# Kernel tuning notes

Measured on AMD Instinct MI355X. Metric: run time of the kernel, lower is better.

Reference implementation:

```python
import jax, jax.numpy as jnp
import numpy as np

EMBED_DIM = 2048
NUM_HEADS = 16
B, L = 1, 4096


def setup_inputs() -> dict:
    key = jax.random.key(0)
    ks = jax.random.split(key, 6)
    s = 1.0 / np.sqrt(EMBED_DIM)
    return {
        "hidden_states": jax.random.normal(ks[0], (B, L, EMBED_DIM), jnp.float32),
        "Wq": jax.random.normal(ks[1], (EMBED_DIM, EMBED_DIM), jnp.float32) * s,
        "bq": jnp.zeros((EMBED_DIM,), jnp.float32),
        "Wk": jax.random.normal(ks[2], (EMBED_DIM, EMBED_DIM), jnp.float32) * s,
        "bk": jnp.zeros((EMBED_DIM,), jnp.float32),
        "Wv": jax.random.normal(ks[3], (EMBED_DIM, EMBED_DIM), jnp.float32) * s,
        "bv": jnp.zeros((EMBED_DIM,), jnp.float32),
        "Wo": jax.random.normal(ks[4], (EMBED_DIM, EMBED_DIM), jnp.float32) * s,
        "bo": jnp.zeros((EMBED_DIM,), jnp.float32),
        "is_causal": 1,
    }


def reference(hidden_states, Wq, bq, Wk, bk, Wv, bv, Wo, bo, is_causal):
    Bc, Lc, D = hidden_states.shape
    H = NUM_HEADS
    Dh = D // H
    scale = Dh ** (-0.5)

    def proj(W, b):
        # torch Linear: x @ W.T + b; reshape to [B, H, L, Dh]
        y = jnp.einsum('bld,ed->ble', hidden_states, W) + b
        return y.reshape(Bc, Lc, H, Dh).transpose(0, 2, 1, 3)

    q = proj(Wq, bq)
    k = proj(Wk, bk)
    v = proj(Wv, bv)

    scores = jnp.einsum('bhqd,bhkd->bhqk', q, k) * scale  # [B,H,L,L]
    if is_causal:
        causal = jnp.triu(jnp.ones((Lc, Lc), dtype=bool), k=1)
        scores = jnp.where(causal, -jnp.inf, scores)
    w = jax.nn.softmax(scores, axis=-1)
    attn = jnp.einsum('bhqk,bhkd->bhqd', w, v)
    attn = attn.transpose(0, 2, 1, 3).reshape(Bc, Lc, D)
    return jnp.einsum('bld,ed->ble', attn, Wo) + bo
```

## Files before the change

### kernel.cpp

```cpp
#include <hip/hip_runtime.h>
#include <hip/hip_bf16.h>

typedef unsigned short u16;
typedef unsigned int u32;
typedef __attribute__((ext_vector_type(8))) short short8;
typedef __attribute__((ext_vector_type(4))) float f32x4;

#define L 4096
#define DMODEL 2048
#define NHEADS 16
#define DHEAD 128
#define QSCALE (0.08838834764831845f * 1.44269504088896340f)

__device__ __forceinline__ u16 f2bf(float f){
  union { float f; unsigned int i; } v; v.f = f;
  unsigned int u = v.i;
  u += 0x7fffu + ((u >> 16) & 1u);
  return (u16)(u >> 16);
}

__device__ __forceinline__ u32 cvtpk(float lo, float hi){
  u32 d;
  asm("v_cvt_pk_bf16_f32 %0, %1, %2" : "=v"(d) : "v"(lo), "v"(hi));
  return d;
}

__global__ void cast_all_kernel(const float* __restrict__ X, u16* __restrict__ Xo,
                                const float* __restrict__ w0, const float* __restrict__ w1,
                                const float* __restrict__ w2, const float* __restrict__ w3,
                                u16* __restrict__ o0, u16* __restrict__ o1,
                                u16* __restrict__ o2, u16* __restrict__ o3){
  const int y = blockIdx.y;
  const float* in = (y == 0) ? X : (y == 1) ? w0 : (y == 2) ? w1 : (y == 3) ? w2 : w3;
  u16* out = (y == 0) ? Xo : (y == 1) ? o0 : (y == 2) ? o1 : (y == 3) ? o2 : o3;
  const int n = (y == 0) ? (L * DMODEL) : (DMODEL * DMODEL);
  int stride = gridDim.x * blockDim.x * 4;
  for (int j = (blockIdx.x * blockDim.x + threadIdx.x) * 4; j < n; j += stride){
    float4 f = *reinterpret_cast<const float4*>(in + j);
    ushort4 o;
    o.x = f2bf(f.x); o.y = f2bf(f.y); o.z = f2bf(f.z); o.w = f2bf(f.w);
    *reinterpret_cast<ushort4*>(out + j) = o;
  }
}

__device__ __forceinline__ void gl_lds16(void* lds, const void* g){
  __builtin_amdgcn_global_load_lds(
      (const __attribute__((address_space(1))) unsigned int*)g,
      (__attribute__((address_space(3))) unsigned int*)lds, 16, 0, 0);
}

#define GBUF (24576)

__global__ __launch_bounds__(512, 2) void gemm_qkv(const u16* __restrict__ A,
    const u16* __restrict__ Wq, const u16* __restrict__ Wk, const u16* __restrict__ Wv,
    const float* __restrict__ bq, const float* __restrict__ bk, const float* __restrict__ bv,
    u16* __restrict__ Qb, u16* __restrict__ Kb, u16* __restrict__ Vtb){
  extern __shared__ u16 gsm[];
  const int tid = threadIdx.x;
  const int wid = tid >> 6, lane = tid & 63;
  const int wm = wid >> 2, wn = wid & 3;
  const int g = lane >> 4, r = lane & 15;
  const int bx = blockIdx.x;
  const int sel = blockIdx.y >> 4;
  const int byl = blockIdx.y & 15;

  const u16* W      = (sel == 0) ? Wq : (sel == 1) ? Wk : Wv;
  const float* bias = (sel == 0) ? bq : (sel == 1) ? bk : bv;
  const float cscale = (sel == 0) ? QSCALE : 1.0f;

  const int srow = tid >> 3;
  const int sc = ((tid & 7) * 16) ^ ((srow & 7) << 4);
  const u16* Ag = A + ((size_t)(bx * 256) + srow) * DMODEL + (sc >> 1);
  const u16* Bg = W + ((size_t)(byl * 128) + srow) * DMODEL + (sc >> 1);
  const int ldsw = wid * 1024;

  f32x4 acc[8][2];
  #pragma unroll
  for (int m = 0; m < 8; ++m){ acc[m][0] = (f32x4){0,0,0,0}; acc[m][1] = (f32x4){0,0,0,0}; }

  const int NK = DMODEL / 64;

  auto STAGE = [&](int b, int tk){
    char* ab = (char*)(gsm + b * GBUF);
    char* bb = (char*)(gsm + b * GBUF + 16384);
    const int ke = tk * 64;
    #pragma unroll
    for (int i = 0; i < 4; ++i)
      gl_lds16(ab + i * 8192 + ldsw, (const char*)(Ag + (size_t)i * 64 * DMODEL + ke));
    #pragma unroll
    for (int i = 0; i < 2; ++i)
      gl_lds16(bb + i * 8192 + ldsw, (const char*)(Bg + (size_t)i * 64 * DMODEL + ke));
  };

  STAGE(0, 0); STAGE(1, 1);

  for (int t = 0; t < NK; ++t){
    if (t < NK - 1) asm volatile("s_waitcnt vmcnt(6)" ::: "memory");
    else            asm volatile("s_waitcnt vmcnt(0)" ::: "memory");
    __builtin_amdgcn_sched_barrier(0);
    __builtin_amdgcn_s_barrier();
    __builtin_amdgcn_sched_barrier(0);

    if (t + 2 < NK) STAGE((t + 2) % 3, t + 2);

    const char* ab = (const char*)(gsm + (t % 3) * GBUF);
    const char* bb = (const char*)(gsm + (t % 3) * GBUF + 16384);

    short8 af[8][2], bf[2][2];
    #pragma unroll
    for (int mt = 0; mt < 8; ++mt){
      const int ar = wm * 128 + mt * 16 + r;
      #pragma unroll
      for (int ks = 0; ks < 2; ++ks)
        af[mt][ks] = *reinterpret_cast<const short8*>(
            ab + ar * 128 + ((ks * 64 + g * 16) ^ ((ar & 7) << 4)));
    }
    #pragma unroll
    for (int nt = 0; nt < 2; ++nt){
      const int br = wn * 32 + nt * 16 + r;
      #pragma unroll
      for (int ks = 0; ks < 2; ++ks)
        bf[nt][ks] = *reinterpret_cast<const short8*>(
            bb + br * 128 + ((ks * 64 + g * 16) ^ ((br & 7) << 4)));
    }

    __builtin_amdgcn_s_setprio(1);
    #pragma unroll
    for (int mt = 0; mt < 8; ++mt)
      #pragma unroll
      for (int nt = 0; nt < 2; ++nt)
        #pragma unroll
        for (int ks = 0; ks < 2; ++ks)
          acc[mt][nt] = __builtin_amdgcn_mfma_f32_16x16x32_bf16(af[mt][ks], bf[nt][ks], acc[mt][nt], 0, 0, 0);
    __builtin_amdgcn_s_setprio(0);
  }

  #pragma unroll
  for (int nt = 0; nt < 2; ++nt){
    const int col = byl * 128 + wn * 32 + nt * 16 + r;
    const float bv = bias[col];
    #pragma unroll
    for (int mt = 0; mt < 8; ++mt){
      #pragma unroll
      for (int qi = 0; qi < 4; ++qi){
        const int row = bx * 256 + wm * 128 + mt * 16 + g * 4 + qi;
        const u16 hb = f2bf((acc[mt][nt][qi] + bv) * cscale);
        if (sel < 2){
          u16* outp = (sel == 0) ? Qb : Kb;
          outp[(size_t)(col >> 7) * (L * DHEAD) + (size_t)row * DHEAD + (col & 127)] = hb;
        } else {
          Vtb[(size_t)(col >> 7) * (DHEAD * L) + (size_t)(col & 127) * L + row] = hb;
        }
      }
    }
  }
}

__global__ __launch_bounds__(512, 2) void gemm_o(const u16* __restrict__ A, const u16* __restrict__ W,
                                                 const float* __restrict__ bias, float* __restrict__ outp){
  extern __shared__ u16 gsm[];
  const int tid = threadIdx.x;
  const int wid = tid >> 6, lane = tid & 63;
  const int wm = wid >> 2, wn = wid & 3;
  const int g = lane >> 4, r = lane & 15;
  const int bx = blockIdx.x, by = blockIdx.y;

  const int srow = tid >> 3;
  const int sc = ((tid & 7) * 16) ^ ((srow & 7) << 4);
  const u16* Ag = A + ((size_t)(bx * 256) + srow) * DMODEL + (sc >> 1);
  const u16* Bg = W + ((size_t)(by * 128) + srow) * DMODEL + (sc >> 1);
  const int ldsw = wid * 1024;

  f32x4 acc[8][2];
  #pragma unroll
  for (int m = 0; m < 8; ++m){ acc[m][0] = (f32x4){0,0,0,0}; acc[m][1] = (f32x4){0,0,0,0}; }

  const int NK = DMODEL / 64;

  auto STAGE = [&](int b, int tk){
    char* ab = (char*)(gsm + b * GBUF);
    char* bb = (char*)(gsm + b * GBUF + 16384);
    const int ke = tk * 64;
    #pragma unroll
    for (int i = 0; i < 4; ++i)
      gl_lds16(ab + i * 8192 + ldsw, (const char*)(Ag + (size_t)i * 64 * DMODEL + ke));
    #pragma unroll
    for (int i = 0; i < 2; ++i)
      gl_lds16(bb + i * 8192 + ldsw, (const char*)(Bg + (size_t)i * 64 * DMODEL + ke));
  };

  STAGE(0, 0); STAGE(1, 1);

  for (int t = 0; t < NK; ++t){
    if (t < NK - 1) asm volatile("s_waitcnt vmcnt(6)" ::: "memory");
    else            asm volatile("s_waitcnt vmcnt(0)" ::: "memory");
    __builtin_amdgcn_sched_barrier(0);
    __builtin_amdgcn_s_barrier();
    __builtin_amdgcn_sched_barrier(0);

    if (t + 2 < NK) STAGE((t + 2) % 3, t + 2);

    const char* ab = (const char*)(gsm + (t % 3) * GBUF);
    const char* bb = (const char*)(gsm + (t % 3) * GBUF + 16384);

    short8 af[8][2], bf[2][2];
    #pragma unroll
    for (int mt = 0; mt < 8; ++mt){
      const int ar = wm * 128 + mt * 16 + r;
      #pragma unroll
      for (int ks = 0; ks < 2; ++ks)
        af[mt][ks] = *reinterpret_cast<const short8*>(
            ab + ar * 128 + ((ks * 64 + g * 16) ^ ((ar & 7) << 4)));
    }
    #pragma unroll
    for (int nt = 0; nt < 2; ++nt){
      const int br = wn * 32 + nt * 16 + r;
      #pragma unroll
      for (int ks = 0; ks < 2; ++ks)
        bf[nt][ks] = *reinterpret_cast<const short8*>(
            bb + br * 128 + ((ks * 64 + g * 16) ^ ((br & 7) << 4)));
    }

    __builtin_amdgcn_s_setprio(1);
    #pragma unroll
    for (int mt = 0; mt < 8; ++mt)
      #pragma unroll
      for (int nt = 0; nt < 2; ++nt)
        #pragma unroll
        for (int ks = 0; ks < 2; ++ks)
          acc[mt][nt] = __builtin_amdgcn_mfma_f32_16x16x32_bf16(af[mt][ks], bf[nt][ks], acc[mt][nt], 0, 0, 0);
    __builtin_amdgcn_s_setprio(0);
  }

  #pragma unroll
  for (int nt = 0; nt < 2; ++nt){
    const int col = by * 128 + wn * 32 + nt * 16 + r;
    const float bv = bias[col];
    #pragma unroll
    for (int mt = 0; mt < 8; ++mt){
      #pragma unroll
      for (int qi = 0; qi < 4; ++qi){
        const int row = bx * 256 + wm * 128 + mt * 16 + g * 4 + qi;
        outp[(size_t)row * DMODEL + col] = acc[mt][nt][qi] + bv;
      }
    }
  }
}


__device__ __forceinline__ void stage_K64(u16* buf, const u16* Kh, int kv0, int wid, int lane){
  #pragma unroll
  for (int i = 0; i < 4; ++i){
    int ib = (wid * 4 + i) * 1024;
    int off = ib + lane * 16;
    int row = off >> 8;
    int c = off & 255;
    int sc = c ^ ((row & 7) << 4);
    gl_lds16((char*)buf + ib, (const char*)(Kh + (size_t)(kv0 + row) * DHEAD) + sc);
  }
}

__device__ __forceinline__ void stage_V64(u16* buf, const u16* Vh, int kv0, int wid, int lane){
  #pragma unroll
  for (int i = 0; i < 4; ++i){
    int ib = (wid * 4 + i) * 1024;
    int off = ib + lane * 16;
    int row = off >> 7;
    int c = off & 127;
    int sc = c ^ ((row & 7) << 4);
    gl_lds16((char*)buf + ib, (const char*)(Vh + (size_t)row * L + kv0) + sc);
  }
}

__device__ __forceinline__ void sm_R(f32x4 (&s)[4], float &l, bool dg, int qrow,
                                     int kv0, int g, u32 (&paw)[2][4]){
  if (dg){
    #pragma unroll
    for (int cb = 0; cb < 4; ++cb){
      int kvb = kv0 + cb * 16 + g * 4;
      #pragma unroll
      for (int e = 0; e < 4; ++e)
        if (kvb + e > qrow) s[cb][e] = -1e30f;
    }
  }
  float rs = 0.f;
  u32 pk[4][2];
  #pragma unroll
  for (int cb = 0; cb < 4; ++cb){
    float p0 = __builtin_amdgcn_exp2f(s[cb][0]);
    float p1 = __builtin_amdgcn_exp2f(s[cb][1]);
    float p2 = __builtin_amdgcn_exp2f(s[cb][2]);
    float p3 = __builtin_amdgcn_exp2f(s[cb][3]);
    rs += (p0 + p1) + (p2 + p3);
    pk[cb][0] = cvtpk(p0, p1);
    pk[cb][1] = cvtpk(p2, p3);
  }
  rs += __shfl_xor(rs, 16);
  rs += __shfl_xor(rs, 32);
  l += rs;
  #pragma unroll
  for (int ks = 0; ks < 2; ++ks){
    #pragma unroll
    for (int h = 0; h < 2; ++h){
      u32 a = pk[ks * 2][h], b = pk[ks * 2 + 1][h];
      asm volatile("v_permlane32_swap_b32 %0, %1" : "+v"(a), "+v"(b));
      asm volatile("v_permlane16_swap_b32 %0, %1" : "+v"(a), "+v"(b));
      paw[ks][h] = a;
      paw[ks][2 + h] = b;
    }
  }
}

__global__ __launch_bounds__(256, 2) void attn_kernel(const u16* __restrict__ Q, const u16* __restrict__ Km,
                                                      const u16* __restrict__ Vt, u16* __restrict__ Ob,
                                                      const int* __restrict__ is_causal_p){
  extern __shared__ u16 smem[];
  u16* Ks  = smem;
  u16* Vsm = smem + 16384;

  const int lane = threadIdx.x & 63, wid = threadIdx.x >> 6;
  const int g = lane >> 4, r = lane & 15;

  int lg = (blockIdx.x & 7) * 64 + (blockIdx.x >> 3);
  int head = lg >> 5;
  int raw = lg & 31;
  int j = (head & 1) ? (31 - raw) : raw;
  const int jA = j, jB = 63 - j;
  const int causal = *is_causal_p;
  const int nt = causal ? (jB + 1) : 64;

  const u16* Qh = Q  + (size_t)head * L * DHEAD;
  const u16* Kh = Km + (size_t)head * L * DHEAD;
  const u16* Vh = Vt + (size_t)head * DHEAD * L;

  const int rowA = 64 * jA + wid * 16;
  const int rowB = 64 * jB + wid * 16;

  short8 qf[2][4];
  #pragma unroll
  for (int kb = 0; kb < 4; ++kb){
    qf[0][kb] = *reinterpret_cast<const short8*>(&Qh[(size_t)(rowA + r) * DHEAD + kb * 32 + g * 8]);
    qf[1][kb] = *reinterpret_cast<const short8*>(&Qh[(size_t)(rowB + r) * DHEAD + kb * 32 + g * 8]);
  }

  f32x4 o[2][8];
  #pragma unroll
  for (int m = 0; m < 2; ++m)
    #pragma unroll
    for (int db = 0; db < 8; ++db) o[m][db] = (f32x4){0.f, 0.f, 0.f, 0.f};
  float lA = 0.f, lB = 0.f;

  stage_K64(Ks,  Kh, 0, wid, lane);
  stage_V64(Vsm, Vh, 0, wid, lane);

  for (int t = 0; t < nt; ++t){
    const int kv0 = t * 64;
    const bool actA = (!causal) || (t <= jA);
    const bool dgA = causal && (t == jA);
    const bool dgB = causal && (t == jB);

    asm volatile("s_waitcnt vmcnt(0)" ::: "memory");
    __builtin_amdgcn_sched_barrier(0);
    __builtin_amdgcn_s_barrier();
    __builtin_amdgcn_sched_barrier(0);

    if (t + 1 < nt){
      stage_K64(Ks  + ((t + 1) & 1) * 8192, Kh, kv0 + 64, wid, lane);
      stage_V64(Vsm + ((t + 1) & 1) * 8192, Vh, kv0 + 64, wid, lane);
    }

    const char* Kb = (const char*)(Ks  + (t & 1) * 8192);
    const char* Vb = (const char*)(Vsm + (t & 1) * 8192);

    f32x4 s[2][4];
    #pragma unroll
    for (int m = 0; m < 2; ++m)
      #pragma unroll
      for (int cb = 0; cb < 4; ++cb) s[m][cb] = (f32x4){-16.f, -16.f, -16.f, -16.f};
    __builtin_amdgcn_s_setprio(1);
    #pragma unroll
    for (int cb = 0; cb < 4; ++cb){
      const int rr = cb * 16 + r;
      short8 kf[4];
      #pragma unroll
      for (int kb = 0; kb < 4; ++kb)
        kf[kb] = *reinterpret_cast<const short8*>(
            Kb + rr * 256 + ((kb * 64 + g * 16) ^ ((rr & 7) << 4)));
      if (actA){
        #pragma unroll
        for (int kb = 0; kb < 4; ++kb)
          s[0][cb] = __builtin_amdgcn_mfma_f32_16x16x32_bf16(kf[kb], qf[0][kb], s[0][cb], 0, 0, 0);
      }
      #pragma unroll
      for (int kb = 0; kb < 4; ++kb)
        s[1][cb] = __builtin_amdgcn_mfma_f32_16x16x32_bf16(kf[kb], qf[1][kb], s[1][cb], 0, 0, 0);
    }
    __builtin_amdgcn_s_setprio(0);

    u32 pawA[2][4], pawB[2][4];
    if (actA) sm_R(s[0], lA, dgA, rowA + r, kv0, g, pawA);
    sm_R(s[1], lB, dgB, rowB + r, kv0, g, pawB);

    __builtin_amdgcn_s_setprio(1);
    #pragma unroll
    for (int st = 0; st < 2; ++st){
      union { u32 u[4]; short8 v; } pa0, pa1;
      #pragma unroll
      for (int w = 0; w < 4; ++w){ pa0.u[w] = pawA[st][w]; pa1.u[w] = pawB[st][w]; }
      #pragma unroll
      for (int db = 0; db < 8; ++db){
        const int rv = db * 16 + r;
        short8 vf = *reinterpret_cast<const short8*>(
            Vb + rv * 128 + (((st * 32 + g * 8) * 2) ^ ((rv & 7) << 4)));
        if (actA)
          o[0][db] = __builtin_amdgcn_mfma_f32_16x16x32_bf16(pa0.v, vf, o[0][db], 0, 0, 0);
        o[1][db] = __builtin_amdgcn_mfma_f32_16x16x32_bf16(pa1.v, vf, o[1][db], 0, 0, 0);
      }
    }
    __builtin_amdgcn_s_setprio(0);
  }

  #pragma unroll
  for (int m = 0; m < 2; ++m){
    const int rbase = m ? rowB : rowA;
    const float lv = m ? lB : lA;
    float lb[4];
    #pragma unroll
    for (int qi = 0; qi < 4; ++qi) lb[qi] = __shfl(lv, g * 4 + qi);
    #pragma unroll
    for (int db = 0; db < 8; ++db)
      #pragma unroll
      for (int qi = 0; qi < 4; ++qi){
        float val = o[m][db][qi] / lb[qi];
        int qrow = rbase + g * 4 + qi;
        Ob[(size_t)qrow * DMODEL + head * DHEAD + db * 16 + r] = f2bf(val);
      }
  }
}

extern "C" void kernel_launch(void* const* d_in, const int* in_sizes, int n_in,
                              void* d_out, int out_size, void* d_ws, size_t ws_size,
                              hipStream_t stream){
  const float* X  = (const float*)d_in[0];
  const float* Wq = (const float*)d_in[1];
  const float* bq = (const float*)d_in[2];
  const float* Wk = (const float*)d_in[3];
  const float* bk = (const float*)d_in[4];
  const float* Wv = (const float*)d_in[5];
  const float* bv = (const float*)d_in[6];
  const float* Wo = (const float*)d_in[7];
  const float* bo = (const float*)d_in[8];
  const int*   isc = (const int*)d_in[9];

  char* ws = (char*)d_ws;
  u16* Xb  = (u16*)(ws);
  u16* Qb  = (u16*)(ws + 16777216);
  u16* Kb  = (u16*)(ws + 33554432);
  u16* Vtb = (u16*)(ws + 50331648);
  u16* Wqb = (u16*)(ws + 67108864);
  u16* Wkb = (u16*)(ws + 75497472);
  u16* Wvb = (u16*)(ws + 83886080);
  u16* Wob = (u16*)(ws + 92274688);
  u16* Ob  = Xb;

  (void)hipFuncSetAttribute(reinterpret_cast<const void*>(attn_kernel),
                            hipFuncAttributeMaxDynamicSharedMemorySize, 65536);
  (void)hipFuncSetAttribute(reinterpret_cast<const void*>(gemm_qkv),
                            hipFuncAttributeMaxDynamicSharedMemorySize, 147456);
  (void)hipFuncSetAttribute(reinterpret_cast<const void*>(gemm_o),
                            hipFuncAttributeMaxDynamicSharedMemorySize, 147456);

  cast_all_kernel<<<dim3(1024, 5), 256, 0, stream>>>(X, Xb, Wq, Wk, Wv, Wo,
                                                     Wqb, Wkb, Wvb, Wob);

  gemm_qkv<<<dim3(16, 48), 512, 147456, stream>>>(Xb, Wqb, Wkb, Wvb, bq, bk, bv, Qb, Kb, Vtb);

  attn_kernel<<<512, 256, 65536, stream>>>(Qb, Kb, Vtb, Ob, isc);

  gemm_o<<<dim3(16, 16), 512, 147456, stream>>>(Ob, Wob, bo, (float*)d_out);
}
```

Measured before the change: 293.1 us.

## Retile projection GEMMs to 128x128 tiles with K=32 and block swizzle

Replaces the 256x128 tile, 512-thread, K=64 GEMMs for the QKV and output projections with a shared templated 128x128 tile, 256-thread, K=32 kernel. It uses a three-stage pipeline in about 48KB of LDS and remaps block IDs so that each group of 8 consecutive blocks is spread across the grid, aiming for better L2 locality across XCDs. The goal is more blocks and higher occupancy (launch bounds 256,3) for a better wave count on the GPU. The cost is lower per-block data reuse, more loop iterations with barriers, and a narrower LDS swizzle that may cause bank conflicts.

```diff
diff --git a/kernel.cpp b/kernel.cpp
--- a/kernel.cpp
+++ b/kernel.cpp
@@ -49,202 +49,135 @@
       (__attribute__((address_space(3))) unsigned int*)lds, 16, 0, 0);
 }
 
-#define GBUF (24576)
-
-__global__ __launch_bounds__(512, 2) void gemm_qkv(const u16* __restrict__ A,
+#define GBUF 8192
+
+template<int MODE>
+__device__ __forceinline__ void gemm128(const u16* __restrict__ A, const u16* __restrict__ W,
+                                        const float* __restrict__ bias, void* __restrict__ outp,
+                                        float cscale, int bx, int by, u16* gsm){
+  const int tid = threadIdx.x;
+  const int wid = tid >> 6, lane = tid & 63;
+  const int wm = wid >> 1, wn = wid & 1;
+  const int g = lane >> 4, r = lane & 15;
+
+  const int srow = tid >> 2;
+  const int sc = ((tid & 3) * 16) ^ (((srow >> 1) & 3) << 4);
+  const u16* Ag = A + ((size_t)(bx * 128) + srow) * DMODEL + (sc >> 1);
+  const u16* Bg = W + ((size_t)(by * 128) + srow) * DMODEL + (sc >> 1);
+
+  f32x4 acc[4][4];
+  #pragma unroll
+  for (int m = 0; m < 4; ++m)
+    #pragma unroll
+    for (int n = 0; n < 4; ++n) acc[m][n] = (f32x4){0,0,0,0};
+
+  const int NK = DMODEL / 32;
+
+  auto STAGE = [&](int b, int tk){
+    char* ab = (char*)(gsm + b * GBUF);
+    char* bb = (char*)(gsm + b * GBUF + 4096);
+    const int ke = tk * 32;
+    #pragma unroll
+    for (int i = 0; i < 2; ++i)
+      gl_lds16(ab + i * 4096 + tid * 16 - lane * 16 + lane * 16 - tid * 16 + tid * 16,
+               (const char*)(Ag + (size_t)(i * 64) * DMODEL + ke));
+    #pragma unroll
+    for (int i = 0; i < 2; ++i)
+      gl_lds16(bb + i * 4096 + tid * 16,
+               (const char*)(Bg + (size_t)(i * 64) * DMODEL + ke));
+  };
+
+  STAGE(0, 0); STAGE(1, 1);
+
+  int cur = 0;
+  for (int t = 0; t < NK; ++t){
+    if (t < NK - 1) asm volatile("s_waitcnt vmcnt(4)" ::: "memory");
+    else            asm volatile("s_waitcnt vmcnt(0)" ::: "memory");
+    __builtin_amdgcn_sched_barrier(0);
+    __builtin_amdgcn_s_barrier();
+    __builtin_amdgcn_sched_barrier(0);
+
+    if (t + 2 < NK){
+      int nb = cur + 2; if (nb >= 3) nb -= 3;
+      STAGE(nb, t + 2);
+    }
+
+    const char* ab = (const char*)(gsm + cur * GBUF);
+    const char* bb = (const char*)(gsm + cur * GBUF + 4096);
+
+    short8 af[4], bf[4];
+    #pragma unroll
+    for (int mt = 0; mt < 4; ++mt){
+      const int ar = wm * 64 + mt * 16 + r;
+      af[mt] = *reinterpret_cast<const short8*>(
+          ab + ar * 64 + ((g * 16) ^ (((ar >> 1) & 3) << 4)));
+    }
+    #pragma unroll
+    for (int nt = 0; nt < 4; ++nt){
+      const int br = wn * 64 + nt * 16 + r;
+      bf[nt] = *reinterpret_cast<const short8*>(
+          bb + br * 64 + ((g * 16) ^ (((br >> 1) & 3) << 4)));
+    }
+
+    __builtin_amdgcn_s_setprio(1);
+    #pragma unroll
+    for (int mt = 0; mt < 4; ++mt)
+      #pragma unroll
+      for (int nt = 0; nt < 4; ++nt)
+        acc[mt][nt] = __builtin_amdgcn_mfma_f32_16x16x32_bf16(af[mt], bf[nt], acc[mt][nt], 0, 0, 0);
+    __builtin_amdgcn_s_setprio(0);
+
+    ++cur; if (cur == 3) cur = 0;
+  }
+
+  #pragma unroll
+  for (int nt = 0; nt < 4; ++nt){
+    const int col = by * 128 + wn * 64 + nt * 16 + r;
+    const float bv = bias[col & (DMODEL - 1)];
+    #pragma unroll
+    for (int mt = 0; mt < 4; ++mt){
+      #pragma unroll
+      for (int qi = 0; qi < 4; ++qi){
+        const int row = bx * 128 + wm * 64 + mt * 16 + g * 4 + qi;
+        if (MODE == 0){
+          ((u16*)outp)[(size_t)((col & (DMODEL-1)) >> 7) * (L * DHEAD) + (size_t)row * DHEAD + (col & 127)]
+              = f2bf((acc[mt][nt][qi] + bv) * cscale);
+        } else if (MODE == 1){
+          ((u16*)outp)[(size_t)((col & (DMODEL-1)) >> 7) * (DHEAD * L) + (size_t)(col & 127) * L + row]
+              = f2bf(acc[mt][nt][qi] + bv);
+        } else {
+          ((float*)outp)[(size_t)row * DMODEL + col] = acc[mt][nt][qi] + bv;
+        }
+      }
+    }
+  }
+}
+
+__global__ __launch_bounds__(256, 3) void gemm_qkv(const u16* __restrict__ A,
     const u16* __restrict__ Wq, const u16* __restrict__ Wk, const u16* __restrict__ Wv,
     const float* __restrict__ bq, const float* __restrict__ bk, const float* __restrict__ bv,
     u16* __restrict__ Qb, u16* __restrict__ Kb, u16* __restrict__ Vtb){
   extern __shared__ u16 gsm[];
-  const int tid = threadIdx.x;
-  const int wid = tid >> 6, lane = tid & 63;
-  const int wm = wid >> 2, wn = wid & 3;
-  const int g = lane >> 4, r = lane & 15;
-  const int bx = blockIdx.x;
-  const int sel = blockIdx.y >> 4;
-  const int byl = blockIdx.y & 15;
-
+  int id = blockIdx.x;
+  int nid = (id & 7) * 192 + (id >> 3);
+  int by = nid >> 5, bx = nid & 31;
+  int sel = by >> 4, byl = by & 15;
   const u16* W      = (sel == 0) ? Wq : (sel == 1) ? Wk : Wv;
   const float* bias = (sel == 0) ? bq : (sel == 1) ? bk : bv;
-  const float cscale = (sel == 0) ? QSCALE : 1.0f;
-
-  const int srow = tid >> 3;
-  const int sc = ((tid & 7) * 16) ^ ((srow & 7) << 4);
-  const u16* Ag = A + ((size_t)(bx * 256) + srow) * DMODEL + (sc >> 1);
-  const u16* Bg = W + ((size_t)(byl * 128) + srow) * DMODEL + (sc >> 1);
-  const int ldsw = wid * 1024;
-
-  f32x4 acc[8][2];
-  #pragma unroll
-  for (int m = 0; m < 8; ++m){ acc[m][0] = (f32x4){0,0,0,0}; acc[m][1] = (f32x4){0,0,0,0}; }
-
-  const int NK = DMODEL / 64;
-
-  auto STAGE = [&](int b, int tk){
-    char* ab = (char*)(gsm + b * GBUF);
-    char* bb = (char*)(gsm + b * GBUF + 16384);
-    const int ke = tk * 64;
-    #pragma unroll
-    for (int i = 0; i < 4; ++i)
-      gl_lds16(ab + i * 8192 + ldsw, (const char*)(Ag + (size_t)i * 64 * DMODEL + ke));
-    #pragma unroll
-    for (int i = 0; i < 2; ++i)
-      gl_lds16(bb + i * 8192 + ldsw, (const char*)(Bg + (size_t)i * 64 * DMODEL + ke));
-  };
-
-  STAGE(0, 0); STAGE(1, 1);
-
-  for (int t = 0; t < NK; ++t){
-    if (t < NK - 1) asm volatile("s_waitcnt vmcnt(6)" ::: "memory");
-    else            asm volatile("s_waitcnt vmcnt(0)" ::: "memory");
-    __builtin_amdgcn_sched_barrier(0);
-    __builtin_amdgcn_s_barrier();
-    __builtin_amdgcn_sched_barrier(0);
-
-    if (t + 2 < NK) STAGE((t + 2) % 3, t + 2);
-
-    const char* ab = (const char*)(gsm + (t % 3) * GBUF);
-    const char* bb = (const char*)(gsm + (t % 3) * GBUF + 16384);
-
-    short8 af[8][2], bf[2][2];
-    #pragma unroll
-    for (int mt = 0; mt < 8; ++mt){
-      const int ar = wm * 128 + mt * 16 + r;
-      #pragma unroll
-      for (int ks = 0; ks < 2; ++ks)
-        af[mt][ks] = *reinterpret_cast<const short8*>(
-            ab + ar * 128 + ((ks * 64 + g * 16) ^ ((ar & 7) << 4)));
-    }
-    #pragma unroll
-    for (int nt = 0; nt < 2; ++nt){
-      const int br = wn * 32 + nt * 16 + r;
-      #pragma unroll
-      for (int ks = 0; ks < 2; ++ks)
-        bf[nt][ks] = *reinterpret_cast<const short8*>(
-            bb + br * 128 + ((ks * 64 + g * 16) ^ ((br & 7) << 4)));
-    }
-
-    __builtin_amdgcn_s_setprio(1);
-    #pragma unroll
-    for (int mt = 0; mt < 8; ++mt)
-      #pragma unroll
-      for (int nt = 0; nt < 2; ++nt)
-        #pragma unroll
-        for (int ks = 0; ks < 2; ++ks)
-          acc[mt][nt] = __builtin_amdgcn_mfma_f32_16x16x32_bf16(af[mt][ks], bf[nt][ks], acc[mt][nt], 0, 0, 0);
-    __builtin_amdgcn_s_setprio(0);
-  }
-
-  #pragma unroll
-  for (int nt = 0; nt < 2; ++nt){
-    const int col = byl * 128 + wn * 32 + nt * 16 + r;
-    const float bv = bias[col];
-    #pragma unroll
-    for (int mt = 0; mt < 8; ++mt){
-      #pragma unroll
-      for (int qi = 0; qi < 4; ++qi){
-        const int row = bx * 256 + wm * 128 + mt * 16 + g * 4 + qi;
-        const u16 hb = f2bf((acc[mt][nt][qi] + bv) * cscale);
-        if (sel < 2){
-          u16* outp = (sel == 0) ? Qb : Kb;
-          outp[(size_t)(col >> 7) * (L * DHEAD) + (size_t)row * DHEAD + (col & 127)] = hb;
-        } else {
-          Vtb[(size_t)(col >> 7) * (DHEAD * L) + (size_t)(col & 127) * L + row] = hb;
-        }
-      }
-    }
-  }
-}
-
-__global__ __launch_bounds__(512, 2) void gemm_o(const u16* __restrict__ A, const u16* __restrict__ W,
+  if (sel < 2)
+    gemm128<0>(A, W, bias, (sel == 0) ? (void*)Qb : (void*)Kb,
+               (sel == 0) ? QSCALE : 1.0f, bx, byl, gsm);
+  else
+    gemm128<1>(A, W, bias, (void*)Vtb, 1.0f, bx, byl, gsm);
+}
+
+__global__ __launch_bounds__(256, 3) void gemm_o(const u16* __restrict__ A, const u16* __restrict__ W,
                                                  const float* __restrict__ bias, float* __restrict__ outp){
   extern __shared__ u16 gsm[];
-  const int tid = threadIdx.x;
-  const int wid = tid >> 6, lane = tid & 63;
-  const int wm = wid >> 2, wn = wid & 3;
-  const int g = lane >> 4, r = lane & 15;
-  const int bx = blockIdx.x, by = blockIdx.y;
-
-  const int srow = tid >> 3;
-  const int sc = ((tid & 7) * 16) ^ ((srow & 7) << 4);
-  const u16* Ag = A + ((size_t)(bx * 256) + srow) * DMODEL + (sc >> 1);
-  const u16* Bg = W + ((size_t)(by * 128) + srow) * DMODEL + (sc >> 1);
-  const int ldsw = wid * 1024;
-
-  f32x4 acc[8][2];
-  #pragma unroll
-  for (int m = 0; m < 8; ++m){ acc[m][0] = (f32x4){0,0,0,0}; acc[m][1] = (f32x4){0,0,0,0}; }
-
-  const int NK = DMODEL / 64;
-
-  auto STAGE = [&](int b, int tk){
-    char* ab = (char*)(gsm + b * GBUF);
-    char* bb = (char*)(gsm + b * GBUF + 16384);
-    const int ke = tk * 64;
-    #pragma unroll
-    for (int i = 0; i < 4; ++i)
-      gl_lds16(ab + i * 8192 + ldsw, (const char*)(Ag + (size_t)i * 64 * DMODEL + ke));
-    #pragma unroll
-    for (int i = 0; i < 2; ++i)
-      gl_lds16(bb + i * 8192 + ldsw, (const char*)(Bg + (size_t)i * 64 * DMODEL + ke));
-  };
-
-  STAGE(0, 0); STAGE(1, 1);
-
-  for (int t = 0; t < NK; ++t){
-    if (t < NK - 1) asm volatile("s_waitcnt vmcnt(6)" ::: "memory");
-    else            asm volatile("s_waitcnt vmcnt(0)" ::: "memory");
-    __builtin_amdgcn_sched_barrier(0);
-    __builtin_amdgcn_s_barrier();
-    __builtin_amdgcn_sched_barrier(0);
-
-    if (t + 2 < NK) STAGE((t + 2) % 3, t + 2);
-
-    const char* ab = (const char*)(gsm + (t % 3) * GBUF);
-    const char* bb = (const char*)(gsm + (t % 3) * GBUF + 16384);
-
-    short8 af[8][2], bf[2][2];
-    #pragma unroll
-    for (int mt = 0; mt < 8; ++mt){
-      const int ar = wm * 128 + mt * 16 + r;
-      #pragma unroll
-      for (int ks = 0; ks < 2; ++ks)
-        af[mt][ks] = *reinterpret_cast<const short8*>(
-            ab + ar * 128 + ((ks * 64 + g * 16) ^ ((ar & 7) << 4)));
-    }
-    #pragma unroll
-    for (int nt = 0; nt < 2; ++nt){
-      const int br = wn * 32 + nt * 16 + r;
-      #pragma unroll
-      for (int ks = 0; ks < 2; ++ks)
-        bf[nt][ks] = *reinterpret_cast<const short8*>(
-            bb + br * 128 + ((ks * 64 + g * 16) ^ ((br & 7) << 4)));
-    }
-
-    __builtin_amdgcn_s_setprio(1);
-    #pragma unroll
-    for (int mt = 0; mt < 8; ++mt)
-      #pragma unroll
-      for (int nt = 0; nt < 2; ++nt)
-        #pragma unroll
-        for (int ks = 0; ks < 2; ++ks)
-          acc[mt][nt] = __builtin_amdgcn_mfma_f32_16x16x32_bf16(af[mt][ks], bf[nt][ks], acc[mt][nt], 0, 0, 0);
-    __builtin_amdgcn_s_setprio(0);
-  }
-
-  #pragma unroll
-  for (int nt = 0; nt < 2; ++nt){
-    const int col = by * 128 + wn * 32 + nt * 16 + r;
-    const float bv = bias[col];
-    #pragma unroll
-    for (int mt = 0; mt < 8; ++mt){
-      #pragma unroll
-      for (int qi = 0; qi < 4; ++qi){
-        const int row = bx * 256 + wm * 128 + mt * 16 + g * 4 + qi;
-        outp[(size_t)row * DMODEL + col] = acc[mt][nt][qi] + bv;
-      }
-    }
-  }
+  int id = blockIdx.x;
+  int nid = (id & 7) * 64 + (id >> 3);
+  int by = nid >> 5, bx = nid & 31;
+  gemm128<2>(A, W, bias, (void*)outp, 1.0f, bx, by, gsm);
 }
 
 
@@ -466,16 +399,16 @@
   (void)hipFuncSetAttribute(reinterpret_cast<const void*>(attn_kernel),
                             hipFuncAttributeMaxDynamicSharedMemorySize, 65536);
   (void)hipFuncSetAttribute(reinterpret_cast<const void*>(gemm_qkv),
-                            hipFuncAttributeMaxDynamicSharedMemorySize, 147456);
+                            hipFuncAttributeMaxDynamicSharedMemorySize, 49152);
   (void)hipFuncSetAttribute(reinterpret_cast<const void*>(gemm_o),
-                            hipFuncAttributeMaxDynamicSharedMemorySize, 147456);
+                            hipFuncAttributeMaxDynamicSharedMemorySize, 49152);
 
   cast_all_kernel<<<dim3(1024, 5), 256, 0, stream>>>(X, Xb, Wq, Wk, Wv, Wo,
                                                      Wqb, Wkb, Wvb, Wob);
 
-  gemm_qkv<<<dim3(16, 48), 512, 147456, stream>>>(Xb, Wqb, Wkb, Wvb, bq, bk, bv, Qb, Kb, Vtb);
+  gemm_qkv<<<1536, 256, 49152, stream>>>(Xb, Wqb, Wkb, Wvb, bq, bk, bv, Qb, Kb, Vtb);
 
   attn_kernel<<<512, 256, 65536, stream>>>(Qb, Kb, Vtb, Ob, isc);
 
-  gemm_o<<<dim3(16, 16), 512, 147456, stream>>>(Ob, Wob, bo, (float*)d_out);
-}
+  gemm_o<<<512, 256, 49152, stream>>>(Ob, Wob, bo, (float*)d_out);
+}
```

Measured after the change: 309.3 us. 1.06x slower.
